# Kernel optimization log

Hardware: AMD Instinct MI355X
Metric: run time of the kernel (lower is better)

## Reference

```python
import jax, jax.numpy as jnp
import numpy as np

BATCH = 1      # a
SEQ = 512      # b == h == num_query
DIM = 128      # c
N_HEADS = BATCH * SEQ  # n = 512, required by the module's view(n, c, h) contract


def setup_inputs() -> dict:
    key = jax.random.key(0)
    ks = jax.random.split(key, 9)
    s = 0.02  # small init scale for weights
    shp = (BATCH, SEQ, SEQ, DIM)
    return {
        "query": jax.random.normal(ks[0], shp, jnp.float32),
        "key": jax.random.normal(ks[1], shp, jnp.float32),
        "value": jax.random.normal(ks[2], shp, jnp.float32),
        "Wq": jax.random.normal(ks[3], (DIM, DIM), jnp.float32) * s,
        "bq": jax.random.normal(ks[4], (DIM,), jnp.float32) * s,
        "Wk": jax.random.normal(ks[5], (DIM, DIM), jnp.float32) * s,
        "bk": jax.random.normal(ks[6], (DIM,), jnp.float32) * s,
        "Wv": jax.random.normal(ks[7], (DIM, DIM), jnp.float32) * s,
        "bv": jax.random.normal(ks[8], (DIM,), jnp.float32) * s,
    }


def reference(query, key, value, Wq, bq, Wk, bk, Wv, bv):
    n, c = N_HEADS, DIM
    h = query.shape[1]  # SEQ

    def proj(x, W, b):
        # torch Linear: x @ W.T + b, then view(n, c, h).transpose(-2,-1).unsqueeze(1)
        y = x @ W.T + b                       # (a, b, b, c)
        y = y.reshape(n, c, h)                # row-major reshape, same as torch .view
        return jnp.swapaxes(y, -2, -1)[:, None]  # (n, 1, h, c)

    q = proj(query, Wq, bq)
    k = proj(key, Wk, bk)
    v = proj(value, Wv, bv)

    attn = (q @ jnp.swapaxes(k, -1, -2)) / jnp.sqrt(jnp.float32(c))  # (n,1,h,h)
    attn = jax.nn.softmax(attn, axis=-1)
    # dropout p=0.66 is identity in eval mode
    ctxt = (attn @ v)[:, 0]  # (n, h, c)

    batch_size, num_query = query.shape[0], query.shape[1]
    output = ctxt.reshape(batch_size, num_query, h * c)  # (a, b, b*c)
    return output, attn
```

## Files before the change

### kernel.cpp

```cpp
#include <hip/hip_runtime.h>
#include <stdint.h>

typedef float f32x4 __attribute__((ext_vector_type(4)));
typedef short s16x8 __attribute__((ext_vector_type(8)));
typedef short s16x4 __attribute__((ext_vector_type(4)));

#define MFMA16(a, b, c) __builtin_amdgcn_mfma_f32_16x16x32_bf16(a, b, c, 0, 0, 0)

__device__ __forceinline__ unsigned short f2bf(float f) {
  union { float f; uint32_t u; } v; v.f = f;
  return (unsigned short)((v.u + 0x7FFFu + ((v.u >> 16) & 1u)) >> 16);
}
__device__ __forceinline__ float bf2f(unsigned short s) {
  union { float f; uint32_t u; } v; v.u = ((uint32_t)s) << 16;
  return v.f;
}
__device__ __forceinline__ s16x8 cvt8(const float* p) {
  f32x4 a = *(const f32x4*)p;
  f32x4 b = *(const f32x4*)(p + 4);
  s16x8 t;
  t[0] = (short)f2bf(a[0]); t[1] = (short)f2bf(a[1]);
  t[2] = (short)f2bf(a[2]); t[3] = (short)f2bf(a[3]);
  t[4] = (short)f2bf(b[0]); t[5] = (short)f2bf(b[1]);
  t[6] = (short)f2bf(b[2]); t[7] = (short)f2bf(b[3]);
  return t;
}
template <int N> __device__ __forceinline__ void vmwait() {
  asm volatile("s_waitcnt vmcnt(%0)" ::"i"(N) : "memory");
}
__device__ __forceinline__ void blockbar() {
  __builtin_amdgcn_s_barrier();
  asm volatile("" ::: "memory");
}
__device__ __forceinline__ void gl_lds16(const void* g, void* l) {
  __builtin_amdgcn_global_load_lds((const __attribute__((address_space(1))) void*)g,
                                   (__attribute__((address_space(3))) void*)l, 16, 0, 0);
}

__global__ __launch_bounds__(256) void proj_kernel(
    const float* __restrict__ Xq, const float* __restrict__ Xk, const float* __restrict__ Xv,
    const float* __restrict__ Wq, const float* __restrict__ bq,
    const float* __restrict__ Wk, const float* __restrict__ bk,
    const float* __restrict__ Wv, const float* __restrict__ bv,
    unsigned short* __restrict__ Qt, unsigned short* __restrict__ Kt,
    unsigned short* __restrict__ Vf) {
  __shared__ unsigned char Wsh[32768];

  const int ty = blockIdx.y;
  const float* X = (ty == 0) ? Xq : (ty == 1) ? Xk : Xv;
  const float* W = (ty == 0) ? Wq : (ty == 1) ? Wk : Wv;
  const float* B = (ty == 0) ? bq : (ty == 1) ? bk : bv;
  unsigned short* out = (ty == 0) ? Qt : (ty == 1) ? Kt : Vf;
  const bool transposed = (ty != 2);

  const int tid = threadIdx.x;
  const int lane = tid & 63;
  const int wave = tid >> 6;
  const int l15 = lane & 15;
  const int g = lane >> 4;

  {
    const int r = tid >> 1;
    const int cb = (tid & 1) * 64;
    const float* wp = W + (size_t)r * 128 + cb;
#pragma unroll
    for (int c8 = 0; c8 < 8; ++c8) {
      s16x8 w = cvt8(wp + 8 * c8);
      const int byte = r * 256 + ((cb * 2 + c8 * 16) ^ ((r & 7) << 4));
      *(s16x8*)(Wsh + byte) = w;
    }
  }
  __syncthreads();

  auto wfrag = [&](int f, int kc) -> s16x8 {
    const int row = 16 * f + l15;
    return *(const s16x8*)(Wsh + row * 256 + ((64 * kc + 16 * g) ^ ((row & 7) << 4)));
  };

  if (transposed) {
    float bias_s[8];
#pragma unroll
    for (int f = 0; f < 8; ++f) bias_s[f] = B[16 * f + l15];

    auto loadX = [&](s16x8 (&xf)[4], int t) {
      const int jb = blockIdx.x * 512 + t * 64 + wave * 16;
      const int jrow = jb + (l15 >> 2) + 4 * (l15 & 3);
      const float* xr = X + (size_t)jrow * 128 + 8 * g;
#pragma unroll
      for (int kc = 0; kc < 4; ++kc) xf[kc] = cvt8(xr + 32 * kc);
    };
    auto computeStore = [&](s16x8 (&xf)[4], int t) {
      const int jb = blockIdx.x * 512 + t * 64 + wave * 16;
      f32x4 acc[8];
#pragma unroll
      for (int f = 0; f < 8; ++f) acc[f] = (f32x4){0.f, 0.f, 0.f, 0.f};
#pragma unroll
      for (int kc = 0; kc < 4; ++kc)
#pragma unroll
        for (int f = 0; f < 8; ++f) acc[f] = MFMA16(xf[kc], wfrag(f, kc), acc[f]);
      const int n = jb >> 9;
      const int c0 = (jb & 511) >> 2;
#pragma unroll
      for (int f = 0; f < 8; ++f) {
        const int h = 128 * g + 16 * f + l15;
        s16x4 pv;
#pragma unroll
        for (int r = 0; r < 4; ++r) pv[r] = (short)f2bf(acc[f][r] + bias_s[f]);
        *(s16x4*)(out + (size_t)n * 65536 + (size_t)h * 128 + c0) = pv;
      }
    };

    s16x8 xfA[4], xfB[4];
    loadX(xfA, 0);
#pragma unroll
    for (int t = 0; t < 8; ++t) {
      if ((t & 1) == 0) {
        if (t < 7) loadX(xfB, t + 1);
        computeStore(xfA, t);
      } else {
        if (t < 7) loadX(xfA, t + 1);
        computeStore(xfB, t);
      }
    }
  } else {
    f32x4 bias_v[8];
#pragma unroll
    for (int f = 0; f < 8; ++f) bias_v[f] = *(const f32x4*)(B + 16 * f + 4 * g);

    auto loadX = [&](s16x8 (&xf)[4], int t) {
      const int jb = blockIdx.x * 512 + t * 64 + wave * 16;
      const int jrow = jb + l15;
      const float* xr = X + (size_t)jrow * 128 + 8 * g;
#pragma unroll
      for (int kc = 0; kc < 4; ++kc) xf[kc] = cvt8(xr + 32 * kc);
    };
    auto computeStore = [&](s16x8 (&xf)[4], int t) {
      const int jb = blockIdx.x * 512 + t * 64 + wave * 16;
      f32x4 acc[8];
#pragma unroll
      for (int f = 0; f < 8; ++f) acc[f] = (f32x4){0.f, 0.f, 0.f, 0.f};
#pragma unroll
      for (int kc = 0; kc < 4; ++kc)
#pragma unroll
        for (int f = 0; f < 8; ++f) acc[f] = MFMA16(wfrag(f, kc), xf[kc], acc[f]);
      const int j = jb + l15;
#pragma unroll
      for (int f = 0; f < 8; ++f) {
        const int cc0 = 16 * f + 4 * g;
        s16x4 pv;
#pragma unroll
        for (int r = 0; r < 4; ++r) pv[r] = (short)f2bf(acc[f][r] + bias_v[f][r]);
        *(s16x4*)(out + (size_t)j * 128 + cc0) = pv;
      }
    };

    s16x8 xfA[4], xfB[4];
    loadX(xfA, 0);
#pragma unroll
    for (int t = 0; t < 8; ++t) {
      if ((t & 1) == 0) {
        if (t < 7) loadX(xfB, t + 1);
        computeStore(xfA, t);
      } else {
        if (t < 7) loadX(xfA, t + 1);
        computeStore(xfB, t);
      }
    }
  }
}

__global__ __launch_bounds__(256, 2) void fattn_kernel(
    const unsigned short* __restrict__ Qt, const unsigned short* __restrict__ Kt,
    const unsigned short* __restrict__ Vf, float* __restrict__ out0,
    float* __restrict__ attn_out) {
  __shared__ unsigned char Stg[40960];

  const int tid = threadIdx.x;
  const int lane = tid & 63;
  const int wave = tid >> 6;
  const int l15 = lane & 15;
  const int g = lane >> 4;

  const int bid = blockIdx.x;
  const int nb = (bid & 7) * 512 + (bid >> 3);
  const int head = nb >> 3;
  const int h0 = (nb & 7) * 64;
  const float scale = 0.08838834764831845f;

  const size_t khead = (size_t)head * 65536;
  const unsigned short* qbase =
      Qt + khead + (size_t)(h0 + 16 * wave + l15) * 128 + 8 * g;
  s16x8 qf0 = *(const s16x8*)(qbase);
  s16x8 qf1 = *(const s16x8*)(qbase + 32);
  s16x8 qf2 = *(const s16x8*)(qbase + 64);
  s16x8 qf3 = *(const s16x8*)(qbase + 96);

  const int sig = 8 * (l15 >> 2) + (l15 & 3);
  const unsigned short* Kh = Kt + khead;
  const unsigned short* Vh = Vf + khead;

  auto stageK = [&](int w) {
#pragma unroll
    for (int j = 0; j < 2; ++j) {
      const int i = 2 * wave + j;
      const int cl = i >> 2, kc = i & 3;
      const unsigned short* src =
          Kh + (size_t)sig * 128 + 8 * g + (size_t)w * 4096 + cl * 512 + 32 * kc;
      gl_lds16(src, Stg + (w % 5) * 8192 + i * 1024);
    }
  };
  auto stageV = [&](int w) {
#pragma unroll
    for (int j = 0; j < 2; ++j) {
      const int i = 2 * wave + j;
      const int half = i >> 2, fi = i & 3;
      const unsigned short* src =
          Vh + (size_t)l15 * 512 + 8 * g + half * 32768 + w * 32 + (size_t)fi * 8192;
      gl_lds16(src, Stg + (w % 5) * 8192 + i * 1024);
    }
  };

  const int lb = lane * 16;
  s16x8 st0, st1, st2, st3, st4, st5, st6, st7;
  s16x8 st8, st9, st10, st11, st12, st13, st14, st15;
  float rs = 0.f;

#define WINDOW_A(W, ST)                                              \
  do {                                                               \
    const unsigned char* kb8 = Stg + ((W) % 5) * 8192;               \
    s16x8 ka0 = *(const s16x8*)(kb8 + lb);                           \
    s16x8 ka1 = *(const s16x8*)(kb8 + 1024 + lb);                    \
    s16x8 ka2 = *(const s16x8*)(kb8 + 2048 + lb);                    \
    s16x8 ka3 = *(const s16x8*)(kb8 + 3072 + lb);                    \
    s16x8 kb0 = *(const s16x8*)(kb8 + 4096 + lb);                    \
    s16x8 kb1 = *(const s16x8*)(kb8 + 5120 + lb);                    \
    s16x8 kb2 = *(const s16x8*)(kb8 + 6144 + lb);                    \
    s16x8 kb3 = *(const s16x8*)(kb8 + 7168 + lb);                    \
    f32x4 sA = {0.f, 0.f, 0.f, 0.f}, sB = {0.f, 0.f, 0.f, 0.f};      \
    sA = MFMA16(ka0, qf0, sA); sA = MFMA16(ka1, qf1, sA);            \
    sA = MFMA16(ka2, qf2, sA); sA = MFMA16(ka3, qf3, sA);            \
    sB = MFMA16(kb0, qf0, sB); sB = MFMA16(kb1, qf1, sB);            \
    sB = MFMA16(kb2, qf2, sB); sB = MFMA16(kb3, qf3, sB);            \
    s16x8 fr;                                                        \
    float e;                                                         \
    e = __expf(sA[0] * scale); rs += e; fr[0] = (short)f2bf(e);      \
    e = __expf(sA[1] * scale); rs += e; fr[1] = (short)f2bf(e);      \
    e = __expf(sA[2] * scale); rs += e; fr[2] = (short)f2bf(e);      \
    e = __expf(sA[3] * scale); rs += e; fr[3] = (short)f2bf(e);      \
    e = __expf(sB[0] * scale); rs += e; fr[4] = (short)f2bf(e);      \
    e = __expf(sB[1] * scale); rs += e; fr[5] = (short)f2bf(e);      \
    e = __expf(sB[2] * scale); rs += e; fr[6] = (short)f2bf(e);      \
    e = __expf(sB[3] * scale); rs += e; fr[7] = (short)f2bf(e);      \
    ST = fr;                                                         \
  } while (0)

#define STEPA(W, ST)                                                 \
  do { vmwait<6>(); blockbar(); stageK((W) + 4); WINDOW_A(W, ST); } while (0)

  stageK(0); stageK(1); stageK(2); stageK(3);
  STEPA(0, st0);  STEPA(1, st1);  STEPA(2, st2);  STEPA(3, st3);
  STEPA(4, st4);  STEPA(5, st5);  STEPA(6, st6);  STEPA(7, st7);
  STEPA(8, st8);  STEPA(9, st9);  STEPA(10, st10); STEPA(11, st11);
  vmwait<6>(); blockbar(); WINDOW_A(12, st12);
  vmwait<4>(); blockbar(); WINDOW_A(13, st13);
  vmwait<2>(); blockbar(); WINDOW_A(14, st14);
  vmwait<0>(); blockbar(); WINDOW_A(15, st15);

  rs += __shfl_xor(rs, 16);
  rs += __shfl_xor(rs, 32);
  const float inv = 1.0f / rs;

  blockbar();

  f32x4 acc2[8];
#pragma unroll
  for (int f = 0; f < 8; ++f) acc2[f] = (f32x4){0.f, 0.f, 0.f, 0.f};

#define WINDOW_B(W, ST)                                                    \
  do {                                                                     \
    const s16x8 pc = ST;                                                   \
    const unsigned char* vb8 = Stg + ((W) % 5) * 8192;                     \
    acc2[0] = MFMA16(pc, *(const s16x8*)(vb8 + lb), acc2[0]);              \
    acc2[1] = MFMA16(pc, *(const s16x8*)(vb8 + 1024 + lb), acc2[1]);       \
    acc2[2] = MFMA16(pc, *(const s16x8*)(vb8 + 2048 + lb), acc2[2]);       \
    acc2[3] = MFMA16(pc, *(const s16x8*)(vb8 + 3072 + lb), acc2[3]);       \
    acc2[4] = MFMA16(pc, *(const s16x8*)(vb8 + 4096 + lb), acc2[4]);       \
    acc2[5] = MFMA16(pc, *(const s16x8*)(vb8 + 5120 + lb), acc2[5]);       \
    acc2[6] = MFMA16(pc, *(const s16x8*)(vb8 + 6144 + lb), acc2[6]);       \
    acc2[7] = MFMA16(pc, *(const s16x8*)(vb8 + 7168 + lb), acc2[7]);       \
  } while (0)

#define STEPB(W, ST)                                                 \
  do { vmwait<6>(); blockbar(); stageV((W) + 4); WINDOW_B(W, ST); } while (0)

  stageV(0); stageV(1); stageV(2); stageV(3);
  STEPB(0, st0);  STEPB(1, st1);  STEPB(2, st2);  STEPB(3, st3);
  STEPB(4, st4);  STEPB(5, st5);  STEPB(6, st6);  STEPB(7, st7);
  STEPB(8, st8);  STEPB(9, st9);  STEPB(10, st10); STEPB(11, st11);
  vmwait<6>(); blockbar(); WINDOW_B(12, st12);
  vmwait<4>(); blockbar(); WINDOW_B(13, st13);
  vmwait<2>(); blockbar(); WINDOW_B(14, st14);
  vmwait<0>(); blockbar(); WINDOW_B(15, st15);

  float* ap = attn_out + (size_t)head * 262144 + (size_t)(h0 + 16 * wave + l15) * 512 + 8 * g;

#define OUTW(W, ST)                                                  \
  do {                                                               \
    const s16x8 pc = ST;                                             \
    f32x4 o0, o1;                                                    \
    o0[0] = bf2f((unsigned short)pc[0]) * inv;                       \
    o0[1] = bf2f((unsigned short)pc[1]) * inv;                       \
    o0[2] = bf2f((unsigned short)pc[2]) * inv;                       \
    o0[3] = bf2f((unsigned short)pc[3]) * inv;                       \
    o1[0] = bf2f((unsigned short)pc[4]) * inv;                       \
    o1[1] = bf2f((unsigned short)pc[5]) * inv;                       \
    o1[2] = bf2f((unsigned short)pc[6]) * inv;                       \
    o1[3] = bf2f((unsigned short)pc[7]) * inv;                       \
    *(f32x4*)(ap + (W) * 32) = o0;                                   \
    *(f32x4*)(ap + (W) * 32 + 4) = o1;                               \
  } while (0)

  OUTW(0, st0);  OUTW(1, st1);  OUTW(2, st2);  OUTW(3, st3);
  OUTW(4, st4);  OUTW(5, st5);  OUTW(6, st6);  OUTW(7, st7);
  OUTW(8, st8);  OUTW(9, st9);  OUTW(10, st10); OUTW(11, st11);
  OUTW(12, st12); OUTW(13, st13); OUTW(14, st14); OUTW(15, st15);

  float invm[4];
#pragma unroll
  for (int r = 0; r < 4; ++r) invm[r] = __shfl(inv, 4 * g + r);

  float* op = out0 + khead + (size_t)(h0 + 16 * wave + 4 * g) * 128 + l15;
#pragma unroll
  for (int f = 0; f < 8; ++f)
#pragma unroll
    for (int r = 0; r < 4; ++r)
      __builtin_nontemporal_store(acc2[f][r] * invm[r], op + (size_t)r * 128 + f * 16);
}

extern "C" void kernel_launch(void* const* d_in, const int* in_sizes, int n_in,
                              void* d_out, int out_size, void* d_ws, size_t ws_size,
                              hipStream_t stream) {
  const float* q  = (const float*)d_in[0];
  const float* k  = (const float*)d_in[1];
  const float* v  = (const float*)d_in[2];
  const float* Wq = (const float*)d_in[3];
  const float* bq = (const float*)d_in[4];
  const float* Wk = (const float*)d_in[5];
  const float* bk = (const float*)d_in[6];
  const float* Wv = (const float*)d_in[7];
  const float* bv = (const float*)d_in[8];

  unsigned short* Qt = (unsigned short*)d_ws;
  unsigned short* Kt = Qt + 33554432;
  unsigned short* Vf = Kt + 33554432;
  float* out0 = (float*)d_out;
  float* attn = out0 + 33554432;

  dim3 pgrid(512, 3, 1);
  proj_kernel<<<pgrid, 256, 0, stream>>>(q, k, v, Wq, bq, Wk, bk, Wv, bv, Qt, Kt, Vf);
  fattn_kernel<<<4096, 256, 0, stream>>>(Qt, Kt, Vf, out0, attn);
}
```

Measured before the change: 524.9 us.

## Fuse QK-softmax and PV passes into a single K/V staged pipeline

Merges the two separate sweeps (first over K windows for scores/exp, then over V windows for P·V) into one loop that stages K and V for the same window together and runs both MFMA stages per window. This removes one full pipeline fill/drain and a block barrier, and lets the exp work interleave with P·V MFMAs. In exchange LDS use grows from 40 KB to 64 KB per block with a 4-deep, 3-ahead ring, which may limit two blocks per CU and reduces prefetch depth.

```diff
diff --git a/kernel.cpp b/kernel.cpp
--- a/kernel.cpp
+++ b/kernel.cpp
@@ -173,7 +173,7 @@
     const unsigned short* __restrict__ Qt, const unsigned short* __restrict__ Kt,
     const unsigned short* __restrict__ Vf, float* __restrict__ out0,
     float* __restrict__ attn_out) {
-  __shared__ unsigned char Stg[40960];
+  __shared__ unsigned char Stg[65536];
 
   const int tid = threadIdx.x;
   const int lane = tid & 63;
@@ -199,24 +199,23 @@
   const unsigned short* Kh = Kt + khead;
   const unsigned short* Vh = Vf + khead;
 
-  auto stageK = [&](int w) {
+  auto stageKV = [&](int w) {
+    unsigned char* dst = Stg + (w & 3) * 16384;
 #pragma unroll
     for (int j = 0; j < 2; ++j) {
       const int i = 2 * wave + j;
       const int cl = i >> 2, kc = i & 3;
-      const unsigned short* src =
+      const unsigned short* srcK =
           Kh + (size_t)sig * 128 + 8 * g + (size_t)w * 4096 + cl * 512 + 32 * kc;
-      gl_lds16(src, Stg + (w % 5) * 8192 + i * 1024);
-    }
-  };
-  auto stageV = [&](int w) {
+      gl_lds16(srcK, dst + i * 1024);
+    }
 #pragma unroll
     for (int j = 0; j < 2; ++j) {
       const int i = 2 * wave + j;
       const int half = i >> 2, fi = i & 3;
-      const unsigned short* src =
+      const unsigned short* srcV =
           Vh + (size_t)l15 * 512 + 8 * g + half * 32768 + w * 32 + (size_t)fi * 8192;
-      gl_lds16(src, Stg + (w % 5) * 8192 + i * 1024);
+      gl_lds16(srcV, dst + 8192 + i * 1024);
     }
   };
 
@@ -225,82 +224,63 @@
   s16x8 st8, st9, st10, st11, st12, st13, st14, st15;
   float rs = 0.f;
 
-#define WINDOW_A(W, ST)                                              \
-  do {                                                               \
-    const unsigned char* kb8 = Stg + ((W) % 5) * 8192;               \
-    s16x8 ka0 = *(const s16x8*)(kb8 + lb);                           \
-    s16x8 ka1 = *(const s16x8*)(kb8 + 1024 + lb);                    \
-    s16x8 ka2 = *(const s16x8*)(kb8 + 2048 + lb);                    \
-    s16x8 ka3 = *(const s16x8*)(kb8 + 3072 + lb);                    \
-    s16x8 kb0 = *(const s16x8*)(kb8 + 4096 + lb);                    \
-    s16x8 kb1 = *(const s16x8*)(kb8 + 5120 + lb);                    \
-    s16x8 kb2 = *(const s16x8*)(kb8 + 6144 + lb);                    \
-    s16x8 kb3 = *(const s16x8*)(kb8 + 7168 + lb);                    \
-    f32x4 sA = {0.f, 0.f, 0.f, 0.f}, sB = {0.f, 0.f, 0.f, 0.f};      \
-    sA = MFMA16(ka0, qf0, sA); sA = MFMA16(ka1, qf1, sA);            \
-    sA = MFMA16(ka2, qf2, sA); sA = MFMA16(ka3, qf3, sA);            \
-    sB = MFMA16(kb0, qf0, sB); sB = MFMA16(kb1, qf1, sB);            \
-    sB = MFMA16(kb2, qf2, sB); sB = MFMA16(kb3, qf3, sB);            \
-    s16x8 fr;                                                        \
-    float e;                                                         \
-    e = __expf(sA[0] * scale); rs += e; fr[0] = (short)f2bf(e);      \
-    e = __expf(sA[1] * scale); rs += e; fr[1] = (short)f2bf(e);      \
-    e = __expf(sA[2] * scale); rs += e; fr[2] = (short)f2bf(e);      \
-    e = __expf(sA[3] * scale); rs += e; fr[3] = (short)f2bf(e);      \
-    e = __expf(sB[0] * scale); rs += e; fr[4] = (short)f2bf(e);      \
-    e = __expf(sB[1] * scale); rs += e; fr[5] = (short)f2bf(e);      \
-    e = __expf(sB[2] * scale); rs += e; fr[6] = (short)f2bf(e);      \
-    e = __expf(sB[3] * scale); rs += e; fr[7] = (short)f2bf(e);      \
-    ST = fr;                                                         \
+  f32x4 acc2[8];
+#pragma unroll
+  for (int f = 0; f < 8; ++f) acc2[f] = (f32x4){0.f, 0.f, 0.f, 0.f};
+
+#define WINDOW_F(W, ST)                                                    \
+  do {                                                                     \
+    const unsigned char* kb8 = Stg + ((W) & 3) * 16384;                    \
+    s16x8 ka0 = *(const s16x8*)(kb8 + lb);                                 \
+    s16x8 ka1 = *(const s16x8*)(kb8 + 1024 + lb);                          \
+    s16x8 ka2 = *(const s16x8*)(kb8 + 2048 + lb);                          \
+    s16x8 ka3 = *(const s16x8*)(kb8 + 3072 + lb);                          \
+    s16x8 kb0 = *(const s16x8*)(kb8 + 4096 + lb);                          \
+    s16x8 kb1 = *(const s16x8*)(kb8 + 5120 + lb);                          \
+    s16x8 kb2 = *(const s16x8*)(kb8 + 6144 + lb);                          \
+    s16x8 kb3 = *(const s16x8*)(kb8 + 7168 + lb);                          \
+    f32x4 sA = {0.f, 0.f, 0.f, 0.f}, sB = {0.f, 0.f, 0.f, 0.f};            \
+    sA = MFMA16(ka0, qf0, sA); sA = MFMA16(ka1, qf1, sA);                  \
+    sA = MFMA16(ka2, qf2, sA); sA = MFMA16(ka3, qf3, sA);                  \
+    sB = MFMA16(kb0, qf0, sB); sB = MFMA16(kb1, qf1, sB);                  \
+    sB = MFMA16(kb2, qf2, sB); sB = MFMA16(kb3, qf3, sB);                  \
+    s16x8 fr;                                                              \
+    float e;                                                               \
+    e = __expf(sA[0] * scale); rs += e; fr[0] = (short)f2bf(e);            \
+    e = __expf(sA[1] * scale); rs += e; fr[1] = (short)f2bf(e);            \
+    e = __expf(sA[2] * scale); rs += e; fr[2] = (short)f2bf(e);            \
+    e = __expf(sA[3] * scale); rs += e; fr[3] = (short)f2bf(e);            \
+    e = __expf(sB[0] * scale); rs += e; fr[4] = (short)f2bf(e);            \
+    e = __expf(sB[1] * scale); rs += e; fr[5] = (short)f2bf(e);            \
+    e = __expf(sB[2] * scale); rs += e; fr[6] = (short)f2bf(e);            \
+    e = __expf(sB[3] * scale); rs += e; fr[7] = (short)f2bf(e);            \
+    ST = fr;                                                               \
+    const unsigned char* vb8 = kb8 + 8192;                                 \
+    acc2[0] = MFMA16(fr, *(const s16x8*)(vb8 + lb), acc2[0]);              \
+    acc2[1] = MFMA16(fr, *(const s16x8*)(vb8 + 1024 + lb), acc2[1]);       \
+    acc2[2] = MFMA16(fr, *(const s16x8*)(vb8 + 2048 + lb), acc2[2]);       \
+    acc2[3] = MFMA16(fr, *(const s16x8*)(vb8 + 3072 + lb), acc2[3]);       \
+    acc2[4] = MFMA16(fr, *(const s16x8*)(vb8 + 4096 + lb), acc2[4]);       \
+    acc2[5] = MFMA16(fr, *(const s16x8*)(vb8 + 5120 + lb), acc2[5]);       \
+    acc2[6] = MFMA16(fr, *(const s16x8*)(vb8 + 6144 + lb), acc2[6]);       \
+    acc2[7] = MFMA16(fr, *(const s16x8*)(vb8 + 7168 + lb), acc2[7]);       \
   } while (0)
 
-#define STEPA(W, ST)                                                 \
-  do { vmwait<6>(); blockbar(); stageK((W) + 4); WINDOW_A(W, ST); } while (0)
-
-  stageK(0); stageK(1); stageK(2); stageK(3);
-  STEPA(0, st0);  STEPA(1, st1);  STEPA(2, st2);  STEPA(3, st3);
-  STEPA(4, st4);  STEPA(5, st5);  STEPA(6, st6);  STEPA(7, st7);
-  STEPA(8, st8);  STEPA(9, st9);  STEPA(10, st10); STEPA(11, st11);
-  vmwait<6>(); blockbar(); WINDOW_A(12, st12);
-  vmwait<4>(); blockbar(); WINDOW_A(13, st13);
-  vmwait<2>(); blockbar(); WINDOW_A(14, st14);
-  vmwait<0>(); blockbar(); WINDOW_A(15, st15);
+#define STEPF(W, ST)                                                 \
+  do { vmwait<8>(); blockbar(); stageKV((W) + 3); WINDOW_F(W, ST); } while (0)
+
+  stageKV(0); stageKV(1); stageKV(2);
+  STEPF(0, st0);  STEPF(1, st1);  STEPF(2, st2);  STEPF(3, st3);
+  STEPF(4, st4);  STEPF(5, st5);  STEPF(6, st6);  STEPF(7, st7);
+  STEPF(8, st8);  STEPF(9, st9);  STEPF(10, st10); STEPF(11, st11);
+  STEPF(12, st12);
+  vmwait<8>(); blockbar(); WINDOW_F(13, st13);
+  vmwait<4>(); blockbar(); WINDOW_F(14, st14);
+  vmwait<0>(); blockbar(); WINDOW_F(15, st15);
 
   rs += __shfl_xor(rs, 16);
   rs += __shfl_xor(rs, 32);
   const float inv = 1.0f / rs;
-
-  blockbar();
-
-  f32x4 acc2[8];
-#pragma unroll
-  for (int f = 0; f < 8; ++f) acc2[f] = (f32x4){0.f, 0.f, 0.f, 0.f};
-
-#define WINDOW_B(W, ST)                                                    \
-  do {                                                                     \
-    const s16x8 pc = ST;                                                   \
-    const unsigned char* vb8 = Stg + ((W) % 5) * 8192;                     \
-    acc2[0] = MFMA16(pc, *(const s16x8*)(vb8 + lb), acc2[0]);              \
-    acc2[1] = MFMA16(pc, *(const s16x8*)(vb8 + 1024 + lb), acc2[1]);       \
-    acc2[2] = MFMA16(pc, *(const s16x8*)(vb8 + 2048 + lb), acc2[2]);       \
-    acc2[3] = MFMA16(pc, *(const s16x8*)(vb8 + 3072 + lb), acc2[3]);       \
-    acc2[4] = MFMA16(pc, *(const s16x8*)(vb8 + 4096 + lb), acc2[4]);       \
-    acc2[5] = MFMA16(pc, *(const s16x8*)(vb8 + 5120 + lb), acc2[5]);       \
-    acc2[6] = MFMA16(pc, *(const s16x8*)(vb8 + 6144 + lb), acc2[6]);       \
-    acc2[7] = MFMA16(pc, *(const s16x8*)(vb8 + 7168 + lb), acc2[7]);       \
-  } while (0)
-
-#define STEPB(W, ST)                                                 \
-  do { vmwait<6>(); blockbar(); stageV((W) + 4); WINDOW_B(W, ST); } while (0)
-
-  stageV(0); stageV(1); stageV(2); stageV(3);
-  STEPB(0, st0);  STEPB(1, st1);  STEPB(2, st2);  STEPB(3, st3);
-  STEPB(4, st4);  STEPB(5, st5);  STEPB(6, st6);  STEPB(7, st7);
-  STEPB(8, st8);  STEPB(9, st9);  STEPB(10, st10); STEPB(11, st11);
-  vmwait<6>(); blockbar(); WINDOW_B(12, st12);
-  vmwait<4>(); blockbar(); WINDOW_B(13, st13);
-  vmwait<2>(); blockbar(); WINDOW_B(14, st14);
-  vmwait<0>(); blockbar(); WINDOW_B(15, st15);
 
   float* ap = attn_out + (size_t)head * 262144 + (size_t)(h0 + 16 * wave + l15) * 512 + 8 * g;
 
```

Measured after the change: 545.8 us. 1.04x slower.
